# Kernel tuning notes

Hardware: AMD Instinct MI355X
Metric: run time of the kernel (lower is better)

## Reference

```python
import jax, jax.numpy as jnp
import numpy as np

BN_EPS = 0.001

def conv2d(x, w, b, stride, pad):
    # x: NCHW, w: OIHW
    y = jax.lax.conv_general_dilated(x, w, (stride, stride), [(pad, pad), (pad, pad)],
                                     dimension_numbers=('NCHW', 'OIHW', 'NCHW'))
    return y + b[None, :, None, None]

def up2(x):
    return jnp.repeat(jnp.repeat(x, 2, axis=2), 2, axis=3)

def bn_eval(x, g, b):
    # BatchNorm in eval mode with fresh running stats (mean=0, var=1)
    inv = g / jnp.sqrt(1.0 + BN_EPS)
    return inv[None, :, None, None] * x + b[None, :, None, None]

def setup_inputs() -> dict:
    key = jax.random.key(0)
    ks = jax.random.split(key, 16)
    inp = {}
    inp['x_init'] = jax.random.uniform(ks[0], (8, 3, 1024, 1024), dtype=jnp.float32)
    inp['thresh'] = jax.random.uniform(ks[1], (2,), dtype=jnp.float32)
    inp['sample_w'] = jax.random.normal(ks[2], (3, 3, 4, 4), dtype=jnp.float32) * 0.1
    inp['sample_b'] = jax.random.normal(ks[3], (3,), dtype=jnp.float32) * 0.1
    inp['centers'] = jax.random.uniform(ks[4], (8,), dtype=jnp.float32)
    inp['pool1_w'] = jax.random.normal(ks[5], (3, 3, 2, 2), dtype=jnp.float32) * 0.2
    inp['pool1_b'] = jax.random.normal(ks[6], (3,), dtype=jnp.float32) * 0.1
    inp['pool2_w'] = jax.random.normal(ks[7], (3, 3, 2, 2), dtype=jnp.float32) * 0.2
    inp['pool2_b'] = jax.random.normal(ks[8], (3,), dtype=jnp.float32) * 0.1
    inp['ctx_conv_w'] = jax.random.normal(ks[9], (4, 3, 3, 3, 3), dtype=jnp.float32) * 0.2
    inp['ctx_conv_b'] = jax.random.normal(ks[10], (4, 3), dtype=jnp.float32) * 0.1
    inp['ctx_bn_g'] = jax.random.uniform(ks[11], (4, 3), dtype=jnp.float32) + 0.5
    inp['ctx_bn_b'] = jax.random.normal(ks[12], (4, 3), dtype=jnp.float32) * 0.1
    return inp

def _quant_idx_counts(t, mask, centers):
    # counts[k] = #(elements of t with mask and argmin center == k)
    idx = jnp.argmin((t[..., None] - centers) ** 2, axis=-1)  # same shape as t
    oh = idx[..., None] == jnp.arange(centers.shape[0])
    return jnp.sum((mask[..., None] & oh).astype(jnp.float32), axis=(0, 1, 2, 3))

def reference(x_init, thresh, sample_w, sample_b, centers,
              pool1_w, pool1_b, pool2_w, pool2_b,
              ctx_conv_w, ctx_conv_b, ctx_bn_g, ctx_bn_b):
    # spectral norm of sample conv weight (exact largest singular value)
    sigma = jnp.linalg.svd(sample_w.reshape(sample_w.shape[0], -1), compute_uv=False)[0]
    x = conv2d(x_init, sample_w / sigma, sample_b, 4, 0)  # [B,3,H/4,W/4]
    B, C, H, W = x.shape

    # ContextExtractor: conv_i(relu(bn_i(h))), stride 2 each
    h = x_init
    for i in range(3):
        h = conv2d(jax.nn.relu(bn_eval(h, ctx_bn_g[i], ctx_bn_b[i])), ctx_conv_w[i], ctx_conv_b[i], 2, 1)
    h1 = conv2d(jax.nn.relu(bn_eval(h, ctx_bn_g[3], ctx_bn_b[3])), ctx_conv_w[3], ctx_conv_b[3], 2, 1)
    feat_1 = (jnp.tanh(h) + 1.0) / 2.0    # [B,3,H/8,W/8]
    feat_2 = (jnp.tanh(h1) + 1.0) / 2.0   # [B,3,H/16,W/16]

    th_1, th_2 = thresh[0], thresh[1]
    feat_1_ = up2(feat_1)
    feat_2_ = up2(up2(feat_2))

    p1 = conv2d(x, pool1_w, pool1_b, 2, 0)    # half res
    p2 = conv2d(p1, pool2_w, pool2_b, 2, 0)   # quarter res
    ss_1 = up2(p1)
    ss_2 = up2(up2(p2))

    cond_2 = feat_2_ < th_2
    cond_1 = jnp.logical_and(jnp.logical_not(cond_2), feat_1_ < th_1)
    cond_0 = jnp.logical_not(jnp.logical_or(cond_1, cond_2))
    mask_1 = jnp.logical_and(up2(feat_2) >= th_2, feat_1 < th_1)  # half-res mask for p1
    mask_2 = feat_2 < th_2                                         # quarter-res mask for p2

    xq = jnp.where(cond_1, ss_1, x)
    xq = jnp.where(cond_2, ss_2, xq)

    # soft vector quantization against 8 learned centers
    d = (xq[..., None] - centers) ** 2                 # [B,C,H,W,8]
    soft = jnp.sum(centers * jax.nn.softmax(-d, axis=-1), axis=-1)

    # compression statistics (esti_cr; huffman real_cr omitted - host-side, non-tensor)
    esti_size = (jnp.sum(cond_0.astype(jnp.float32))
                 + jnp.sum(cond_1.astype(jnp.float32)) / 4.0
                 + jnp.sum(cond_2.astype(jnp.float32)) / 16.0)
    esti_cr = (1.0 / 16.0) * esti_size / (H * W * C * B)

    # histogram std over comp_data quantization indices, via masked counts
    counts = (_quant_idx_counts(x, cond_0, centers)
              + _quant_idx_counts(p1, mask_1, centers)
              + _quant_idx_counts(p2, mask_2, centers))
    counts = counts / jnp.sum(counts)
    std = jnp.std(counts, ddof=1)

    return (soft, esti_cr, std)
```

## Files before the change

kernel.cpp:

```cpp
#include <hip/hip_runtime.h>
#include <math.h>


#define SENT -1e30f

#define DSTR 68
#define DPLANE 1292

#define SXSTR 72
#define SXCH  (19 * SXSTR)
#define H0STR 36
#define H0CH  (9 * H0STR)

__device__ __forceinline__ float featf(float h) { return 0.5f * (tanhf(h) + 1.0f); }

__device__ __forceinline__ void dma16(const float* g, float* l) {
    __builtin_amdgcn_global_load_lds((const __attribute__((address_space(1))) void*)g,
                                     (__attribute__((address_space(3))) void*)l,
                                     16, 0, 0);
}

__device__ __forceinline__ void stage19(const float* __restrict__ base,
                                        float* __restrict__ L,
                                        int gr0, int gc0, int S, int t) {
    #pragma unroll
    for (int p = 0; p < 2; p++) {
        int idx = t + 256 * p;
        if (idx < 323) {
            int lr = idx / 17;
            int s  = idx - lr * 17;
            int gr = gr0 + lr;
            int gc = gc0 + 4 * s;
            float4 v;
            if (gr >= 0 && gr < S && gc >= 0 && gc < S)
                v = *(const float4*)(base + (size_t)gr * S + gc);
            else { v.x = SENT; v.y = SENT; v.z = SENT; v.w = SENT; }
            *(float4*)&L[lr * SXSTR + 4 * s] = v;
        }
    }
}

__global__ __launch_bounds__(256) void k_fused01(
    const float* __restrict__ xin,
    const float* __restrict__ sw_g, const float* __restrict__ sb,
    const float* __restrict__ ctxw, const float* __restrict__ ctxb,
    const float* __restrict__ bng, const float* __restrict__ bnb,
    const float* __restrict__ p1w, const float* __restrict__ p1b,
    const float* __restrict__ p2w, const float* __restrict__ p2b,
    float* __restrict__ outX, float* __restrict__ outH1,
    float* __restrict__ outP1, float* __restrict__ outP2)
{
    __shared__ float sx[3 * DPLANE];
    __shared__ float sm[3 * H0CH];

    int t = threadIdx.x, bid = blockIdx.x;
    int tileX = bid & 15, bandY = (bid >> 4) & 63, b = bid >> 10;

    int gr0 = bandY * 16 - 3;
    int gc0 = tileX * 64 - 4;

    {
        int slot0 = t;
        int lr0 = slot0 / 17, cs0 = slot0 - 17 * lr0;
        int slot1 = t + 256;
        int lr1 = slot1 / 17, cs1 = slot1 - 17 * lr1;
        int grA = min(max(gr0 + lr0, 0), 1023);
        int gcA = min(max(gc0 + 4 * cs0, 0), 1020);
        int grB = min(max(gr0 + lr1, 0), 1023);
        int gcB = min(max(gc0 + 4 * cs1, 0), 1020);
        int offA = (grA << 10) + gcA;
        int offB = (grB << 10) + gcB;
        int wbase = t & 192;
        #pragma unroll
        for (int c = 0; c < 3; c++) {
            const float* plane = xin + ((size_t)(b * 3 + c) << 20);
            dma16(plane + offA, &sx[c * DPLANE + 4 * wbase]);
            if (t < 67) dma16(plane + offB, &sx[c * DPLANE + 4 * (256 + wbase)]);
        }
    }
    __syncthreads();

    if (tileX == 0 || bandY == 0) {
        float4 sv; sv.x = SENT; sv.y = SENT; sv.z = SENT; sv.w = SENT;
        if (bandY == 0 && t < 153) {
            int c = t / 51, rem = t - 51 * c;
            int lr = rem / 17, cs = rem - 17 * lr;
            *(float4*)&sx[c * DPLANE + lr * DSTR + 4 * cs] = sv;
        }
        if (tileX == 0 && t >= 192 && t < 249) {
            int u = t - 192;
            int c = u / 19, lr = u - 19 * c;
            *(float4*)&sx[c * DPLANE + lr * DSTR] = sv;
        }
        __syncthreads();
    }

    {
        float inv0[3], bb0[3];
        #pragma unroll
        for (int c = 0; c < 3; c++) { inv0[c] = bng[c] / sqrtf(1.001f); bb0[c] = bnb[c]; }
        #pragma unroll
        for (int p = 0; p < 2; p++) {
            int idx = t + 256 * p;
            if (idx < 297) {
                int lhy = idx / 33;
                int lhx = idx - 33 * lhy;
                bool oob = (bandY == 0 && lhy == 0) || (tileX == 0 && lhx == 0);
                float a0 = ctxb[0], a1 = ctxb[1], a2 = ctxb[2];
                #pragma unroll
                for (int c = 0; c < 3; c++) {
                    const float* basep = &sx[c * DPLANE + 2 * lhy * DSTR + 2 * lhx];
                    float inv = inv0[c], bb = bb0[c];
                    #pragma unroll
                    for (int kh = 0; kh < 3; kh++) {
                        float2 c0 = *(const float2*)(basep + kh * DSTR);
                        float2 c1 = *(const float2*)(basep + kh * DSTR + 2);
                        float t0 = fmaxf(fmaf(inv, c0.y, bb), 0.0f);
                        float t1 = fmaxf(fmaf(inv, c1.x, bb), 0.0f);
                        float t2 = fmaxf(fmaf(inv, c1.y, bb), 0.0f);
                        int wi = c * 9 + kh * 3;
                        a0 = fmaf(ctxw[wi], t0, a0); a0 = fmaf(ctxw[wi + 1], t1, a0); a0 = fmaf(ctxw[wi + 2], t2, a0);
                        a1 = fmaf(ctxw[27 + wi], t0, a1); a1 = fmaf(ctxw[28 + wi], t1, a1); a1 = fmaf(ctxw[29 + wi], t2, a1);
                        a2 = fmaf(ctxw[54 + wi], t0, a2); a2 = fmaf(ctxw[55 + wi], t1, a2); a2 = fmaf(ctxw[56 + wi], t2, a2);
                    }
                }
                int o = lhy * H0STR + lhx;
                if (oob) { a0 = SENT; a1 = SENT; a2 = SENT; }
                sm[o] = a0; sm[H0CH + o] = a1; sm[2 * H0CH + o] = a2;
            }
        }
    }
    __syncthreads();

    if (t < 64) {
        int lx = t & 15, ly = t >> 4;
        const float* w1c = ctxw + 81;
        float a0 = ctxb[3], a1 = ctxb[4], a2 = ctxb[5];
        #pragma unroll
        for (int c = 0; c < 3; c++) {
            float inv = bng[3 + c] / sqrtf(1.001f), bb = bnb[3 + c];
            const float* mb = &sm[c * H0CH + 2 * ly * H0STR + 2 * lx];
            #pragma unroll
            for (int kh = 0; kh < 3; kh++) {
                float2 c0 = *(const float2*)(mb + kh * H0STR);
                float c2v = mb[kh * H0STR + 2];
                float t0 = fmaxf(fmaf(inv, c0.x, bb), 0.0f);
                float t1 = fmaxf(fmaf(inv, c0.y, bb), 0.0f);
                float t2 = fmaxf(fmaf(inv, c2v, bb), 0.0f);
                int wi = c * 9 + kh * 3;
                a0 = fmaf(w1c[wi], t0, a0); a0 = fmaf(w1c[wi + 1], t1, a0); a0 = fmaf(w1c[wi + 2], t2, a0);
                a1 = fmaf(w1c[27 + wi], t0, a1); a1 = fmaf(w1c[28 + wi], t1, a1); a1 = fmaf(w1c[29 + wi], t2, a1);
                a2 = fmaf(w1c[54 + wi], t0, a2); a2 = fmaf(w1c[55 + wi], t1, a2); a2 = fmaf(w1c[56 + wi], t2, a2);
            }
        }
        unsigned o = (unsigned)(b * 3) * 65536u + (unsigned)(bandY * 4 + ly) * 256u + tileX * 16 + lx;
        outH1[o] = a0; outH1[o + 65536u] = a1; outH1[o + 131072u] = a2;
    } else if (t < 128) {
        int tl = t - 64;
        float p00 = 0.f, p01 = 0.f, p02 = 0.f, p11 = 0.f, p12 = 0.f, p22 = 0.f;
        if (tl < 48) {
            float a0 = sw_g[tl], a1 = sw_g[48 + tl], a2 = sw_g[96 + tl];
            p00 = a0 * a0; p01 = a0 * a1; p02 = a0 * a2;
            p11 = a1 * a1; p12 = a1 * a2; p22 = a2 * a2;
        }
        #pragma unroll
        for (int off = 32; off > 0; off >>= 1) {
            p00 += __shfl_down(p00, off); p01 += __shfl_down(p01, off);
            p02 += __shfl_down(p02, off); p11 += __shfl_down(p11, off);
            p12 += __shfl_down(p12, off); p22 += __shfl_down(p22, off);
        }
        float inv_sigma = 0.0f;
        if (tl == 0) {
            float q = (p00 + p11 + p22) * (1.0f / 3.0f);
            float pp1 = p01 * p01 + p02 * p02 + p12 * p12;
            float pp2 = (p00 - q) * (p00 - q) + (p11 - q) * (p11 - q)
                      + (p22 - q) * (p22 - q) + 2.0f * pp1;
            float lam;
            if (pp2 < 1e-30f) lam = q;
            else {
                float pr = sqrtf(pp2 / 6.0f);
                float B00 = (p00 - q) / pr, B01 = p01 / pr, B02 = p02 / pr;
                float B11 = (p11 - q) / pr, B12 = p12 / pr, B22 = (p22 - q) / pr;
                float detB = B00 * (B11 * B22 - B12 * B12)
                           - B01 * (B01 * B22 - B12 * B02)
                           + B02 * (B01 * B12 - B11 * B02);
                float r = fminf(1.0f, fmaxf(-1.0f, 0.5f * detB));
                lam = q + 2.0f * pr * cosf(acosf(r) * (1.0f / 3.0f));
            }
            double G00 = p00, G01 = p01, G02 = p02, G11 = p11, G12 = p12, G22 = p22;
            double c2 = G00 + G11 + G22;
            double c1 = G00 * G11 - G01 * G01 + G00 * G22 - G02 * G02 + G11 * G22 - G12 * G12;
            double c0 = G00 * (G11 * G22 - G12 * G12) - G01 * (G01 * G22 - G12 * G02)
                      + G02 * (G01 * G12 - G11 * G02);
            double L = (double)lam;
            #pragma unroll
            for (int it = 0; it < 2; it++) {
                double pv = ((L - c2) * L + c1) * L - c0;
                double dv = (3.0 * L - 2.0 * c2) * L + c1;
                L -= pv / dv;
            }
            inv_sigma = (float)(1.0 / sqrt(L));
        }
        inv_sigma = __shfl(inv_sigma, 0);

        int xl = tl & 15, yl = tl >> 4;
        float4 r[3][4];
        #pragma unroll
        for (int c = 0; c < 3; c++)
            #pragma unroll
            for (int kh = 0; kh < 4; kh++)
                r[c][kh] = *(const float4*)&sx[c * DPLANE + (4 * yl + 3 + kh) * DSTR + 4 * xl + 4];
        float s0 = 0.f, s1 = 0.f, s2 = 0.f;
        #pragma unroll
        for (int c = 0; c < 3; c++)
            #pragma unroll
            for (int kh = 0; kh < 4; kh++) {
                float4 vv = r[c][kh];
                const float* w0 = &sw_g[(0 * 3 + c) * 16 + kh * 4];
                const float* w1 = &sw_g[(1 * 3 + c) * 16 + kh * 4];
                const float* w2 = &sw_g[(2 * 3 + c) * 16 + kh * 4];
                s0 += w0[0] * vv.x + w0[1] * vv.y + w0[2] * vv.z + w0[3] * vv.w;
                s1 += w1[0] * vv.x + w1[1] * vv.y + w1[2] * vv.z + w1[3] * vv.w;
                s2 += w2[0] * vv.x + w2[1] * vv.y + w2[2] * vv.z + w2[3] * vv.w;
            }
        float x0 = fmaf(s0, inv_sigma, sb[0]);
        float x1 = fmaf(s1, inv_sigma, sb[1]);
        float x2 = fmaf(s2, inv_sigma, sb[2]);
        unsigned o = (unsigned)(b * 3) * 65536u + (unsigned)(bandY * 4 + yl) * 256u + tileX * 16 + xl;
        outX[o] = x0; outX[o + 65536u] = x1; outX[o + 131072u] = x2;

        int sl = 2 * (tl & 7) + 32 * ((tl >> 3) & 1);
        float q0 = p1b[0], q1 = p1b[1], q2 = p1b[2];
        #pragma unroll
        for (int dy = 0; dy < 2; dy++)
            #pragma unroll
            for (int dx = 0; dx < 2; dx++) {
                int src = sl + dx + 16 * dy;
                float vx0 = __shfl(x0, src);
                float vx1 = __shfl(x1, src);
                float vx2 = __shfl(x2, src);
                int wi = dy * 2 + dx;
                q0 = fmaf(p1w[wi], vx0, q0); q0 = fmaf(p1w[4 + wi],  vx1, q0); q0 = fmaf(p1w[8 + wi],  vx2, q0);
                q1 = fmaf(p1w[12 + wi], vx0, q1); q1 = fmaf(p1w[16 + wi], vx1, q1); q1 = fmaf(p1w[20 + wi], vx2, q1);
                q2 = fmaf(p1w[24 + wi], vx0, q2); q2 = fmaf(p1w[28 + wi], vx1, q2); q2 = fmaf(p1w[32 + wi], vx2, q2);
            }
        if (tl < 16) {
            int px = tl & 7, py = tl >> 3;
            unsigned op = (unsigned)(b * 3) * 16384u + (unsigned)(bandY * 2 + py) * 128u + tileX * 8 + px;
            outP1[op] = q0; outP1[op + 16384u] = q1; outP1[op + 32768u] = q2;
        }

        int s2l = 2 * (tl & 3);
        float r0 = p2b[0], r1 = p2b[1], r2 = p2b[2];
        #pragma unroll
        for (int dy = 0; dy < 2; dy++)
            #pragma unroll
            for (int dx = 0; dx < 2; dx++) {
                int src = s2l + dx + 8 * dy;
                float vq0 = __shfl(q0, src);
                float vq1 = __shfl(q1, src);
                float vq2 = __shfl(q2, src);
                int wi = dy * 2 + dx;
                r0 = fmaf(p2w[wi], vq0, r0); r0 = fmaf(p2w[4 + wi],  vq1, r0); r0 = fmaf(p2w[8 + wi],  vq2, r0);
                r1 = fmaf(p2w[12 + wi], vq0, r1); r1 = fmaf(p2w[16 + wi], vq1, r1); r1 = fmaf(p2w[20 + wi], vq2, r1);
                r2 = fmaf(p2w[24 + wi], vq0, r2); r2 = fmaf(p2w[28 + wi], vq1, r2); r2 = fmaf(p2w[32 + wi], vq2, r2);
            }
        if (tl < 4) {
            unsigned op = (unsigned)(b * 3) * 4096u + (unsigned)bandY * 64u + tileX * 4 + tl;
            outP2[op] = r0; outP2[op + 4096u] = r1; outP2[op + 8192u] = r2;
        }
    }
}

__global__ __launch_bounds__(256) void k_fused23(
    const float* __restrict__ h1, float* __restrict__ outF1, float* __restrict__ outF2,
    const float* __restrict__ ctxw, const float* __restrict__ ctxb,
    const float* __restrict__ bng, const float* __restrict__ bnb)
{
    __shared__ float sx[3 * SXCH];
    __shared__ float sm[3 * H0CH];

    int t = threadIdx.x, bid = blockIdx.x;
    int tileX = bid & 3, bandY = (bid >> 2) & 15, b = bid >> 6;

    int gr0 = bandY * 16 - 3;
    int gc0 = tileX * 64 - 4;
    #pragma unroll
    for (int c = 0; c < 3; c++)
        stage19(h1 + (size_t)(b * 3 + c) * 65536, &sx[c * SXCH], gr0, gc0, 256, t);
    __syncthreads();

    {
        const float* w2c = ctxw + 162;
        float inv2[3], bb2[3];
        #pragma unroll
        for (int c = 0; c < 3; c++) { inv2[c] = bng[6 + c] / sqrtf(1.001f); bb2[c] = bnb[6 + c]; }
        #pragma unroll
        for (int p = 0; p < 2; p++) {
            int idx = t + 256 * p;
            if (idx < 297) {
                int lhy = idx / 33;
                int lhx = idx - 33 * lhy;
                bool oob = (bandY == 0 && lhy == 0) || (tileX == 0 && lhx == 0);
                float a0 = ctxb[6], a1 = ctxb[7], a2 = ctxb[8];
                #pragma unroll
                for (int c = 0; c < 3; c++) {
                    const float* basep = &sx[c * SXCH + 2 * lhy * SXSTR + 2 * lhx];
                    float inv = inv2[c], bb = bb2[c];
                    #pragma unroll
                    for (int kh = 0; kh < 3; kh++) {
                        float2 c0 = *(const float2*)(basep + kh * SXSTR);
                        float2 c1 = *(const float2*)(basep + kh * SXSTR + 2);
                        float t0 = fmaxf(fmaf(inv, c0.y, bb), 0.0f);
                        float t1 = fmaxf(fmaf(inv, c1.x, bb), 0.0f);
                        float t2 = fmaxf(fmaf(inv, c1.y, bb), 0.0f);
                        int wi = c * 9 + kh * 3;
                        a0 = fmaf(w2c[wi], t0, a0); a0 = fmaf(w2c[wi + 1], t1, a0); a0 = fmaf(w2c[wi + 2], t2, a0);
                        a1 = fmaf(w2c[27 + wi], t0, a1); a1 = fmaf(w2c[28 + wi], t1, a1); a1 = fmaf(w2c[29 + wi], t2, a1);
                        a2 = fmaf(w2c[54 + wi], t0, a2); a2 = fmaf(w2c[55 + wi], t1, a2); a2 = fmaf(w2c[56 + wi], t2, a2);
                    }
                }
                int o = lhy * H0STR + lhx;
                if (!oob && lhy >= 1 && lhx >= 1) {
                    unsigned fo = (unsigned)(b * 3) * 16384u
                                + (unsigned)(8 * bandY + lhy - 1) * 128u + 32 * tileX + lhx - 1;
                    outF1[fo] = featf(a0); outF1[fo + 16384u] = featf(a1); outF1[fo + 32768u] = featf(a2);
                }
                if (oob) { a0 = SENT; a1 = SENT; a2 = SENT; }
                sm[o] = a0; sm[H0CH + o] = a1; sm[2 * H0CH + o] = a2;
            }
        }
    }
    __syncthreads();

    if (t < 64) {
        int lx = t & 15, ly = t >> 4;
        const float* w3c = ctxw + 243;
        float a0 = ctxb[9], a1 = ctxb[10], a2 = ctxb[11];
        #pragma unroll
        for (int c = 0; c < 3; c++) {
            float inv = bng[9 + c] / sqrtf(1.001f), bb = bnb[9 + c];
            const float* mb = &sm[c * H0CH + 2 * ly * H0STR + 2 * lx];
            #pragma unroll
            for (int kh = 0; kh < 3; kh++) {
                float2 c0 = *(const float2*)(mb + kh * H0STR);
                float c2v = mb[kh * H0STR + 2];
                float t0 = fmaxf(fmaf(inv, c0.x, bb), 0.0f);
                float t1 = fmaxf(fmaf(inv, c0.y, bb), 0.0f);
                float t2 = fmaxf(fmaf(inv, c2v, bb), 0.0f);
                int wi = c * 9 + kh * 3;
                a0 = fmaf(w3c[wi], t0, a0); a0 = fmaf(w3c[wi + 1], t1, a0); a0 = fmaf(w3c[wi + 2], t2, a0);
                a1 = fmaf(w3c[27 + wi], t0, a1); a1 = fmaf(w3c[28 + wi], t1, a1); a1 = fmaf(w3c[29 + wi], t2, a1);
                a2 = fmaf(w3c[54 + wi], t0, a2); a2 = fmaf(w3c[55 + wi], t1, a2); a2 = fmaf(w3c[56 + wi], t2, a2);
            }
        }
        unsigned o = (unsigned)(b * 3) * 4096u + (unsigned)(bandY * 4 + ly) * 64u + tileX * 16 + lx;
        outF2[o] = featf(a0); outF2[o + 4096u] = featf(a1); outF2[o + 8192u] = featf(a2);
    }
}

__device__ __forceinline__ int argmin8(float v, const float* __restrict__ sc) {
    float best = 1e30f; int ki = 0;
    #pragma unroll
    for (int k = 0; k < 8; k++) {
        float df = v - sc[k]; float dk = df * df;
        if (dk < best) { best = dk; ki = k; }
    }
    return ki;
}

__global__ __launch_bounds__(256) void k_final(
    const float* __restrict__ x, const float* __restrict__ f1,
    const float* __restrict__ f2, const float* __restrict__ p1,
    const float* __restrict__ p2, const float* __restrict__ thresh,
    const float* __restrict__ centers, float* __restrict__ out,
    int* __restrict__ partials)
{
    __shared__ int sh[4 * 12];
    int t = threadIdx.x;
    int lane = t & 63;
    int* shW = &sh[12 * (t >> 6)];
    if (lane < 12) shW[lane] = 0;
    float sc[8];
    #pragma unroll
    for (int k = 0; k < 8; k++) sc[k] = centers[k];
    __syncthreads();

    float th1 = thresh[0], th2 = thresh[1];
    int gid = blockIdx.x * 256 + t;
    int xc = gid & 255, y = (gid >> 8) & 255, b = gid >> 16;
    unsigned i2 = (unsigned)(((y >> 1) << 7) + (xc >> 1));
    unsigned i4 = (unsigned)(((y >> 2) << 6) + (xc >> 2));
    bool doM1 = ((y & 1) == 0) && ((xc & 1) == 0);
    bool doM2 = ((y & 3) == 0) && ((xc & 3) == 0);
    int c0n = 0, c1n = 0, c2n = 0;

    #pragma unroll
    for (int c = 0; c < 3; c++) {
        unsigned pc = (unsigned)(b * 3 + c);
        float f1v = f1[pc * 16384u + i2];
        float f2v = f2[pc * 4096u + i4];
        float p1v = p1[pc * 16384u + i2];
        float p2v = p2[pc * 4096u + i4];
        float xv  = x[pc * 65536u + (unsigned)((y << 8) + xc)];
        bool cond2 = f2v < th2;
        bool cond1 = (!cond2) && (f1v < th1);
        bool cond0 = !(cond1 || cond2);
        float xq = cond2 ? p2v : (cond1 ? p1v : xv);

        float d[8]; float dmin = 1e30f;
        #pragma unroll
        for (int k = 0; k < 8; k++) { float df = xq - sc[k]; d[k] = df * df; dmin = fminf(dmin, d[k]); }
        float se = 0.f, sn = 0.f;
        #pragma unroll
        for (int k = 0; k < 8; k++) { float e = __expf(dmin - d[k]); se += e; sn = fmaf(sc[k], e, sn); }
        out[pc * 65536u + (unsigned)((y << 8) + xc)] = sn / se;

        c0n += cond0; c1n += cond1; c2n += cond2;

        if (cond0) atomicAdd(&shW[argmin8(xv, sc)], 1);
        if (doM1 && (f2v >= th2) && (f1v < th1)) atomicAdd(&shW[argmin8(p1v, sc)], 1);
        if (doM2 && cond2) atomicAdd(&shW[argmin8(p2v, sc)], 1);
    }
    #pragma unroll
    for (int off = 32; off > 0; off >>= 1) {
        c0n += __shfl_down(c0n, off);
        c1n += __shfl_down(c1n, off);
        c2n += __shfl_down(c2n, off);
    }
    if (lane == 0) { atomicAdd(&shW[8], c0n); atomicAdd(&shW[9], c1n); atomicAdd(&shW[10], c2n); }
    __syncthreads();
    if (t < 12)
        partials[blockIdx.x * 12 + t] = sh[t] + sh[12 + t] + sh[24 + t] + sh[36 + t];
}

__global__ void k_reduce(const int* __restrict__ partials, float* __restrict__ out2) {
    __shared__ int accs[12];
    int t = threadIdx.x;
    if (t < 12) accs[t] = 0;
    __syncthreads();
    int s[12];
    #pragma unroll
    for (int k = 0; k < 12; k++) s[k] = 0;
    for (int r = t; r < 2048; r += 256) {
        const int* row = partials + r * 12;
        #pragma unroll
        for (int k = 0; k < 12; k++) s[k] += row[k];
    }
    #pragma unroll
    for (int k = 0; k < 12; k++) {
        #pragma unroll
        for (int off = 32; off > 0; off >>= 1) s[k] += __shfl_down(s[k], off);
    }
    if ((t & 63) == 0) {
        #pragma unroll
        for (int k = 0; k < 12; k++) if (s[k]) atomicAdd(&accs[k], s[k]);
    }
    __syncthreads();
    if (t == 0) {
        float cnt0 = (float)accs[8], cnt1 = (float)accs[9], cnt2 = (float)accs[10];
        float esti = cnt0 + cnt1 * 0.25f + cnt2 * 0.0625f;
        float cr = (1.0f / 16.0f) * esti / (256.0f * 256.0f * 3.0f * 8.0f);
        float cs[8]; float tot = 0.0f;
        #pragma unroll
        for (int k = 0; k < 8; k++) { cs[k] = (float)accs[k]; tot += cs[k]; }
        float mean = 0.0f;
        #pragma unroll
        for (int k = 0; k < 8; k++) { cs[k] /= tot; mean += cs[k]; }
        mean *= 0.125f;
        float var = 0.0f;
        #pragma unroll
        for (int k = 0; k < 8; k++) { float df = cs[k] - mean; var += df * df; }
        var *= (1.0f / 7.0f);
        out2[0] = cr;
        out2[1] = sqrtf(var);
    }
}

extern "C" void kernel_launch(void* const* d_in, const int* in_sizes, int n_in,
                              void* d_out, int out_size, void* d_ws, size_t ws_size,
                              hipStream_t stream) {
    const float* x_init   = (const float*)d_in[0];
    const float* thresh   = (const float*)d_in[1];
    const float* sample_w = (const float*)d_in[2];
    const float* sample_b = (const float*)d_in[3];
    const float* centers  = (const float*)d_in[4];
    const float* pool1_w  = (const float*)d_in[5];
    const float* pool1_b  = (const float*)d_in[6];
    const float* pool2_w  = (const float*)d_in[7];
    const float* pool2_b  = (const float*)d_in[8];
    const float* ctx_w    = (const float*)d_in[9];
    const float* ctx_b    = (const float*)d_in[10];
    const float* bn_g     = (const float*)d_in[11];
    const float* bn_b     = (const float*)d_in[12];
    float* out = (float*)d_out;

    float* wsf      = (float*)d_ws;
    int*   partials = (int*)wsf;
    float* bufX     = wsf + 32768;
    float* bufH1    = bufX  + 1572864;
    float* bufP1    = bufH1 + 1572864;
    float* bufP2    = bufP1 + 393216;
    float* bufF1    = bufP2 + 98304;
    float* bufF2    = bufF1 + 393216;

    k_fused01<<<8192, 256, 0, stream>>>(x_init, sample_w, sample_b,
                                        ctx_w, ctx_b, bn_g, bn_b,
                                        pool1_w, pool1_b, pool2_w, pool2_b,
                                        bufX, bufH1, bufP1, bufP2);
    k_fused23<<<512, 256, 0, stream>>>(bufH1, bufF1, bufF2,
                                       ctx_w, ctx_b, bn_g, bn_b);
    k_final<<<2048, 256, 0, stream>>>(bufX, bufF1, bufF2, bufP1, bufP2,
                                      thresh, centers, out, partials);
    k_reduce<<<1, 256, 0, stream>>>(partials, out + 1572864);
}
```

Baseline: 206.5 us.

## Fuse final quantization and reduction into ctx kernel via shared-memory features

Merges k_fused23, k_final and k_reduce into one kernel. The f1/f2 feature maps stay in shared memory instead of making a global round trip, and the last block, found through an atomic counter, does the final reduction. The spectral-norm eigenvalue computation is also moved ahead of the first barrier so it overlaps the DMA staging. This removes two launches and the F1/F2 global traffic, but the final stage now runs on only 512 blocks, which lowers parallelism for the softmax work. It also relies on the counter being reset inside the first kernel.

```diff
diff --git a/kernel.cpp b/kernel.cpp
--- a/kernel.cpp
+++ b/kernel.cpp
@@ -48,13 +48,16 @@
     const float* __restrict__ p1w, const float* __restrict__ p1b,
     const float* __restrict__ p2w, const float* __restrict__ p2b,
     float* __restrict__ outX, float* __restrict__ outH1,
-    float* __restrict__ outP1, float* __restrict__ outP2)
+    float* __restrict__ outP1, float* __restrict__ outP2,
+    int* __restrict__ counter)
 {
     __shared__ float sx[3 * DPLANE];
     __shared__ float sm[3 * H0CH];
 
     int t = threadIdx.x, bid = blockIdx.x;
     int tileX = bid & 15, bandY = (bid >> 4) & 63, b = bid >> 10;
+
+    if (bid == 0 && t == 0) *counter = 0;
 
     int gr0 = bandY * 16 - 3;
     int gc0 = tileX * 64 - 4;
@@ -77,6 +80,55 @@
             dma16(plane + offA, &sx[c * DPLANE + 4 * wbase]);
             if (t < 67) dma16(plane + offB, &sx[c * DPLANE + 4 * (256 + wbase)]);
         }
+    }
+
+    float inv_sigma = 0.0f;
+    if (t >= 64 && t < 128) {
+        int tl = t - 64;
+        float p00 = 0.f, p01 = 0.f, p02 = 0.f, p11 = 0.f, p12 = 0.f, p22 = 0.f;
+        if (tl < 48) {
+            float a0 = sw_g[tl], a1 = sw_g[48 + tl], a2 = sw_g[96 + tl];
+            p00 = a0 * a0; p01 = a0 * a1; p02 = a0 * a2;
+            p11 = a1 * a1; p12 = a1 * a2; p22 = a2 * a2;
+        }
+        #pragma unroll
+        for (int off = 32; off > 0; off >>= 1) {
+            p00 += __shfl_down(p00, off); p01 += __shfl_down(p01, off);
+            p02 += __shfl_down(p02, off); p11 += __shfl_down(p11, off);
+            p12 += __shfl_down(p12, off); p22 += __shfl_down(p22, off);
+        }
+        if (tl == 0) {
+            float q = (p00 + p11 + p22) * (1.0f / 3.0f);
+            float pp1 = p01 * p01 + p02 * p02 + p12 * p12;
+            float pp2 = (p00 - q) * (p00 - q) + (p11 - q) * (p11 - q)
+                      + (p22 - q) * (p22 - q) + 2.0f * pp1;
+            float lam;
+            if (pp2 < 1e-30f) lam = q;
+            else {
+                float pr = sqrtf(pp2 / 6.0f);
+                float B00 = (p00 - q) / pr, B01 = p01 / pr, B02 = p02 / pr;
+                float B11 = (p11 - q) / pr, B12 = p12 / pr, B22 = (p22 - q) / pr;
+                float detB = B00 * (B11 * B22 - B12 * B12)
+                           - B01 * (B01 * B22 - B12 * B02)
+                           + B02 * (B01 * B12 - B11 * B02);
+                float r = fminf(1.0f, fmaxf(-1.0f, 0.5f * detB));
+                lam = q + 2.0f * pr * cosf(acosf(r) * (1.0f / 3.0f));
+            }
+            double G00 = p00, G01 = p01, G02 = p02, G11 = p11, G12 = p12, G22 = p22;
+            double c2 = G00 + G11 + G22;
+            double c1 = G00 * G11 - G01 * G01 + G00 * G22 - G02 * G02 + G11 * G22 - G12 * G12;
+            double c0 = G00 * (G11 * G22 - G12 * G12) - G01 * (G01 * G22 - G12 * G02)
+                      + G02 * (G01 * G12 - G11 * G02);
+            double L = (double)lam;
+            #pragma unroll
+            for (int it = 0; it < 2; it++) {
+                double pv = ((L - c2) * L + c1) * L - c0;
+                double dv = (3.0 * L - 2.0 * c2) * L + c1;
+                L -= pv / dv;
+            }
+            inv_sigma = (float)(1.0 / sqrt(L));
+        }
+        inv_sigma = __shfl(inv_sigma, 0);
     }
     __syncthreads();
 
@@ -157,52 +209,6 @@
         outH1[o] = a0; outH1[o + 65536u] = a1; outH1[o + 131072u] = a2;
     } else if (t < 128) {
         int tl = t - 64;
-        float p00 = 0.f, p01 = 0.f, p02 = 0.f, p11 = 0.f, p12 = 0.f, p22 = 0.f;
-        if (tl < 48) {
-            float a0 = sw_g[tl], a1 = sw_g[48 + tl], a2 = sw_g[96 + tl];
-            p00 = a0 * a0; p01 = a0 * a1; p02 = a0 * a2;
-            p11 = a1 * a1; p12 = a1 * a2; p22 = a2 * a2;
-        }
-        #pragma unroll
-        for (int off = 32; off > 0; off >>= 1) {
-            p00 += __shfl_down(p00, off); p01 += __shfl_down(p01, off);
-            p02 += __shfl_down(p02, off); p11 += __shfl_down(p11, off);
-            p12 += __shfl_down(p12, off); p22 += __shfl_down(p22, off);
-        }
-        float inv_sigma = 0.0f;
-        if (tl == 0) {
-            float q = (p00 + p11 + p22) * (1.0f / 3.0f);
-            float pp1 = p01 * p01 + p02 * p02 + p12 * p12;
-            float pp2 = (p00 - q) * (p00 - q) + (p11 - q) * (p11 - q)
-                      + (p22 - q) * (p22 - q) + 2.0f * pp1;
-            float lam;
-            if (pp2 < 1e-30f) lam = q;
-            else {
-                float pr = sqrtf(pp2 / 6.0f);
-                float B00 = (p00 - q) / pr, B01 = p01 / pr, B02 = p02 / pr;
-                float B11 = (p11 - q) / pr, B12 = p12 / pr, B22 = (p22 - q) / pr;
-                float detB = B00 * (B11 * B22 - B12 * B12)
-                           - B01 * (B01 * B22 - B12 * B02)
-                           + B02 * (B01 * B12 - B11 * B02);
-                float r = fminf(1.0f, fmaxf(-1.0f, 0.5f * detB));
-                lam = q + 2.0f * pr * cosf(acosf(r) * (1.0f / 3.0f));
-            }
-            double G00 = p00, G01 = p01, G02 = p02, G11 = p11, G12 = p12, G22 = p22;
-            double c2 = G00 + G11 + G22;
-            double c1 = G00 * G11 - G01 * G01 + G00 * G22 - G02 * G02 + G11 * G22 - G12 * G12;
-            double c0 = G00 * (G11 * G22 - G12 * G12) - G01 * (G01 * G22 - G12 * G02)
-                      + G02 * (G01 * G12 - G11 * G02);
-            double L = (double)lam;
-            #pragma unroll
-            for (int it = 0; it < 2; it++) {
-                double pv = ((L - c2) * L + c1) * L - c0;
-                double dv = (3.0 * L - 2.0 * c2) * L + c1;
-                L -= pv / dv;
-            }
-            inv_sigma = (float)(1.0 / sqrt(L));
-        }
-        inv_sigma = __shfl(inv_sigma, 0);
-
         int xl = tl & 15, yl = tl >> 4;
         float4 r[3][4];
         #pragma unroll
@@ -272,16 +278,39 @@
     }
 }
 
-__global__ __launch_bounds__(256) void k_fused23(
-    const float* __restrict__ h1, float* __restrict__ outF1, float* __restrict__ outF2,
+__device__ __forceinline__ int argmin8(float v, const float* __restrict__ sc) {
+    float best = 1e30f; int ki = 0;
+    #pragma unroll
+    for (int k = 0; k < 8; k++) {
+        float df = v - sc[k]; float dk = df * df;
+        if (dk < best) { best = dk; ki = k; }
+    }
+    return ki;
+}
+
+__global__ __launch_bounds__(256) void k_fused23f(
+    const float* __restrict__ h1, const float* __restrict__ x,
+    const float* __restrict__ p1, const float* __restrict__ p2,
+    const float* __restrict__ thresh, const float* __restrict__ centers,
     const float* __restrict__ ctxw, const float* __restrict__ ctxb,
-    const float* __restrict__ bng, const float* __restrict__ bnb)
+    const float* __restrict__ bng, const float* __restrict__ bnb,
+    float* __restrict__ out, int* __restrict__ partials,
+    int* __restrict__ counter, float* __restrict__ out2)
 {
     __shared__ float sx[3 * SXCH];
     __shared__ float sm[3 * H0CH];
+    __shared__ float sf1[3 * 256];
+    __shared__ float sf2[3 * 64];
+    __shared__ int sh[4 * 12];
+    __shared__ int accs[12];
+    __shared__ bool s_last;
 
     int t = threadIdx.x, bid = blockIdx.x;
     int tileX = bid & 3, bandY = (bid >> 2) & 15, b = bid >> 6;
+    int lane = t & 63;
+    int* shW = &sh[12 * (t >> 6)];
+    if (lane < 12) shW[lane] = 0;
+    if (t == 0) s_last = false;
 
     int gr0 = bandY * 16 - 3;
     int gc0 = tileX * 64 - 4;
@@ -321,10 +350,9 @@
                     }
                 }
                 int o = lhy * H0STR + lhx;
-                if (!oob && lhy >= 1 && lhx >= 1) {
-                    unsigned fo = (unsigned)(b * 3) * 16384u
-                                + (unsigned)(8 * bandY + lhy - 1) * 128u + 32 * tileX + lhx - 1;
-                    outF1[fo] = featf(a0); outF1[fo + 16384u] = featf(a1); outF1[fo + 32768u] = featf(a2);
+                if (lhy >= 1 && lhx >= 1) {
+                    int fo = (lhy - 1) * 32 + (lhx - 1);
+                    sf1[fo] = featf(a0); sf1[256 + fo] = featf(a1); sf1[512 + fo] = featf(a2);
                 }
                 if (oob) { a0 = SENT; a1 = SENT; a2 = SENT; }
                 sm[o] = a0; sm[H0CH + o] = a1; sm[2 * H0CH + o] = a2;
@@ -354,55 +382,32 @@
                 a2 = fmaf(w3c[54 + wi], t0, a2); a2 = fmaf(w3c[55 + wi], t1, a2); a2 = fmaf(w3c[56 + wi], t2, a2);
             }
         }
-        unsigned o = (unsigned)(b * 3) * 4096u + (unsigned)(bandY * 4 + ly) * 64u + tileX * 16 + lx;
-        outF2[o] = featf(a0); outF2[o + 4096u] = featf(a1); outF2[o + 8192u] = featf(a2);
-    }
-}
-
-__device__ __forceinline__ int argmin8(float v, const float* __restrict__ sc) {
-    float best = 1e30f; int ki = 0;
-    #pragma unroll
-    for (int k = 0; k < 8; k++) {
-        float df = v - sc[k]; float dk = df * df;
-        if (dk < best) { best = dk; ki = k; }
-    }
-    return ki;
-}
-
-__global__ __launch_bounds__(256) void k_final(
-    const float* __restrict__ x, const float* __restrict__ f1,
-    const float* __restrict__ f2, const float* __restrict__ p1,
-    const float* __restrict__ p2, const float* __restrict__ thresh,
-    const float* __restrict__ centers, float* __restrict__ out,
-    int* __restrict__ partials)
-{
-    __shared__ int sh[4 * 12];
-    int t = threadIdx.x;
-    int lane = t & 63;
-    int* shW = &sh[12 * (t >> 6)];
-    if (lane < 12) shW[lane] = 0;
+        sf2[t] = featf(a0); sf2[64 + t] = featf(a1); sf2[128 + t] = featf(a2);
+    }
+    __syncthreads();
+
     float sc[8];
     #pragma unroll
     for (int k = 0; k < 8; k++) sc[k] = centers[k];
-    __syncthreads();
-
     float th1 = thresh[0], th2 = thresh[1];
-    int gid = blockIdx.x * 256 + t;
-    int xc = gid & 255, y = (gid >> 8) & 255, b = gid >> 16;
-    unsigned i2 = (unsigned)(((y >> 1) << 7) + (xc >> 1));
-    unsigned i4 = (unsigned)(((y >> 2) << 6) + (xc >> 2));
-    bool doM1 = ((y & 1) == 0) && ((xc & 1) == 0);
-    bool doM2 = ((y & 3) == 0) && ((xc & 3) == 0);
+    int y0 = bandY * 16, x0r = tileX * 64;
     int c0n = 0, c1n = 0, c2n = 0;
 
     #pragma unroll
-    for (int c = 0; c < 3; c++) {
+    for (int k12 = 0; k12 < 12; k12++) {
+        int idx = t + 256 * k12;
+        int c = idx >> 10;
+        int rem = idx & 1023;
+        int ly2 = rem >> 6, lx2 = rem & 63;
+        int y = y0 + ly2, xg = x0r + lx2;
         unsigned pc = (unsigned)(b * 3 + c);
-        float f1v = f1[pc * 16384u + i2];
-        float f2v = f2[pc * 4096u + i4];
-        float p1v = p1[pc * 16384u + i2];
-        float p2v = p2[pc * 4096u + i4];
-        float xv  = x[pc * 65536u + (unsigned)((y << 8) + xc)];
+
+        float f1v = sf1[(c << 8) + ((ly2 >> 1) << 5) + (lx2 >> 1)];
+        float f2v = sf2[(c << 6) + ((ly2 >> 2) << 4) + (lx2 >> 2)];
+        float p1v = p1[pc * 16384u + (unsigned)(((y >> 1) << 7) + (xg >> 1))];
+        float p2v = p2[pc * 4096u + (unsigned)(((y >> 2) << 6) + (xg >> 2))];
+        float xv  = x[pc * 65536u + (unsigned)((y << 8) + xg)];
+
         bool cond2 = f2v < th2;
         bool cond1 = (!cond2) && (f1v < th1);
         bool cond0 = !(cond1 || cond2);
@@ -414,10 +419,12 @@
         float se = 0.f, sn = 0.f;
         #pragma unroll
         for (int k = 0; k < 8; k++) { float e = __expf(dmin - d[k]); se += e; sn = fmaf(sc[k], e, sn); }
-        out[pc * 65536u + (unsigned)((y << 8) + xc)] = sn / se;
+        out[pc * 65536u + (unsigned)((y << 8) + xg)] = sn / se;
 
         c0n += cond0; c1n += cond1; c2n += cond2;
 
+        bool doM1 = ((y & 1) == 0) && ((xg & 1) == 0);
+        bool doM2 = ((y & 3) == 0) && ((xg & 3) == 0);
         if (cond0) atomicAdd(&shW[argmin8(xv, sc)], 1);
         if (doM1 && (f2v >= th2) && (f1v < th1)) atomicAdd(&shW[argmin8(p1v, sc)], 1);
         if (doM2 && cond2) atomicAdd(&shW[argmin8(p2v, sc)], 1);
@@ -431,49 +438,54 @@
     if (lane == 0) { atomicAdd(&shW[8], c0n); atomicAdd(&shW[9], c1n); atomicAdd(&shW[10], c2n); }
     __syncthreads();
     if (t < 12)
-        partials[blockIdx.x * 12 + t] = sh[t] + sh[12 + t] + sh[24 + t] + sh[36 + t];
-}
-
-__global__ void k_reduce(const int* __restrict__ partials, float* __restrict__ out2) {
-    __shared__ int accs[12];
-    int t = threadIdx.x;
-    if (t < 12) accs[t] = 0;
-    __syncthreads();
-    int s[12];
-    #pragma unroll
-    for (int k = 0; k < 12; k++) s[k] = 0;
-    for (int r = t; r < 2048; r += 256) {
-        const int* row = partials + r * 12;
-        #pragma unroll
-        for (int k = 0; k < 12; k++) s[k] += row[k];
-    }
-    #pragma unroll
-    for (int k = 0; k < 12; k++) {
-        #pragma unroll
-        for (int off = 32; off > 0; off >>= 1) s[k] += __shfl_down(s[k], off);
-    }
-    if ((t & 63) == 0) {
-        #pragma unroll
-        for (int k = 0; k < 12; k++) if (s[k]) atomicAdd(&accs[k], s[k]);
-    }
-    __syncthreads();
+        partials[bid * 12 + t] = sh[t] + sh[12 + t] + sh[24 + t] + sh[36 + t];
+    __syncthreads();
+    __threadfence();
     if (t == 0) {
-        float cnt0 = (float)accs[8], cnt1 = (float)accs[9], cnt2 = (float)accs[10];
-        float esti = cnt0 + cnt1 * 0.25f + cnt2 * 0.0625f;
-        float cr = (1.0f / 16.0f) * esti / (256.0f * 256.0f * 3.0f * 8.0f);
-        float cs[8]; float tot = 0.0f;
-        #pragma unroll
-        for (int k = 0; k < 8; k++) { cs[k] = (float)accs[k]; tot += cs[k]; }
-        float mean = 0.0f;
-        #pragma unroll
-        for (int k = 0; k < 8; k++) { cs[k] /= tot; mean += cs[k]; }
-        mean *= 0.125f;
-        float var = 0.0f;
-        #pragma unroll
-        for (int k = 0; k < 8; k++) { float df = cs[k] - mean; var += df * df; }
-        var *= (1.0f / 7.0f);
-        out2[0] = cr;
-        out2[1] = sqrtf(var);
+        unsigned done = atomicAdd((unsigned*)counter, 1u);
+        s_last = (done == 511u);
+    }
+    __syncthreads();
+
+    if (s_last) {
+        if (t < 12) accs[t] = 0;
+        __syncthreads();
+        int s[12];
+        #pragma unroll
+        for (int k = 0; k < 12; k++) s[k] = 0;
+        for (int r = t; r < 512; r += 256) {
+            int* row = partials + r * 12;
+            #pragma unroll
+            for (int k = 0; k < 12; k++) s[k] += atomicAdd(&row[k], 0);
+        }
+        #pragma unroll
+        for (int k = 0; k < 12; k++) {
+            #pragma unroll
+            for (int off = 32; off > 0; off >>= 1) s[k] += __shfl_down(s[k], off);
+        }
+        if (lane == 0) {
+            #pragma unroll
+            for (int k = 0; k < 12; k++) if (s[k]) atomicAdd(&accs[k], s[k]);
+        }
+        __syncthreads();
+        if (t == 0) {
+            float cnt0 = (float)accs[8], cnt1 = (float)accs[9], cnt2 = (float)accs[10];
+            float esti = cnt0 + cnt1 * 0.25f + cnt2 * 0.0625f;
+            float cr = (1.0f / 16.0f) * esti / (256.0f * 256.0f * 3.0f * 8.0f);
+            float cs[8]; float tot = 0.0f;
+            #pragma unroll
+            for (int k = 0; k < 8; k++) { cs[k] = (float)accs[k]; tot += cs[k]; }
+            float mean = 0.0f;
+            #pragma unroll
+            for (int k = 0; k < 8; k++) { cs[k] /= tot; mean += cs[k]; }
+            mean *= 0.125f;
+            float var = 0.0f;
+            #pragma unroll
+            for (int k = 0; k < 8; k++) { float df = cs[k] - mean; var += df * df; }
+            var *= (1.0f / 7.0f);
+            out2[0] = cr;
+            out2[1] = sqrtf(var);
+        }
     }
 }
 
@@ -497,20 +509,18 @@
 
     float* wsf      = (float*)d_ws;
     int*   partials = (int*)wsf;
+    int*   counter  = partials + 6144;
     float* bufX     = wsf + 32768;
     float* bufH1    = bufX  + 1572864;
     float* bufP1    = bufH1 + 1572864;
     float* bufP2    = bufP1 + 393216;
-    float* bufF1    = bufP2 + 98304;
-    float* bufF2    = bufF1 + 393216;
 
     k_fused01<<<8192, 256, 0, stream>>>(x_init, sample_w, sample_b,
                                         ctx_w, ctx_b, bn_g, bn_b,
                                         pool1_w, pool1_b, pool2_w, pool2_b,
-                                        bufX, bufH1, bufP1, bufP2);
-    k_fused23<<<512, 256, 0, stream>>>(bufH1, bufF1, bufF2,
-                                       ctx_w, ctx_b, bn_g, bn_b);
-    k_final<<<2048, 256, 0, stream>>>(bufX, bufF1, bufF2, bufP1, bufP2,
-                                      thresh, centers, out, partials);
-    k_reduce<<<1, 256, 0, stream>>>(partials, out + 1572864);
+                                        bufX, bufH1, bufP1, bufP2, counter);
+    k_fused23f<<<512, 256, 0, stream>>>(bufH1, bufX, bufP1, bufP2,
+                                        thresh, centers,
+                                        ctx_w, ctx_b, bn_g, bn_b,
+                                        out, partials, counter, out + 1572864);
 }
```

Result: slower. 234.7 us (+13.7%).
